# Kernel tuning notes

Measured on AMD Instinct MI355X. Metric: run time of the kernel, lower is better.

## Reference

```python
import jax, jax.numpy as jnp
import numpy as np

SMOOTH = 1e-05
NUM_CLASSES = 2  # binary segmentation labels {0,1}


def setup_inputs() -> dict:
    key = jax.random.key(0)
    k1, k2 = jax.random.split(key)
    shape = (32, 1, 1024, 1024)
    input = jax.random.normal(k1, shape, dtype=jnp.float32)
    target = jax.random.randint(k2, shape, 0, NUM_CLASSES, dtype=jnp.int32)
    return {"input": input, "target": target}


def reference(input, target):
    # sigmoid probabilities, flattened
    p = jax.nn.sigmoid(input).reshape(-1)
    t_int = target.reshape(-1)
    t = t_int.astype(p.dtype)

    # class-frequency histogram (fixed length -> jit-compatible)
    class_frequencies = jnp.bincount(t_int, length=NUM_CLASSES)
    class_weights = 1.0 / (class_frequencies.astype(p.dtype) + SMOOTH) ** 2
    w = class_weights[t_int]  # gather per-pixel weight

    intersection = jnp.sum(w * p * t)
    denominator = jnp.sum(w * (p * p + t * t))
    dice_loss = 1.0 - (2.0 * intersection + SMOOTH) / (denominator + SMOOTH)
    return dice_loss
```

## Files before the change

kernel.cpp:

```cpp
#include <hip/hip_runtime.h>

#define SMOOTH 1e-5

typedef float f32x4 __attribute__((ext_vector_type(4)));
typedef int   i32x4 __attribute__((ext_vector_type(4)));

__device__ __forceinline__ f32x4 ldnt(const f32x4* p) {
    return __builtin_nontemporal_load(p);
}

__global__ __launch_bounds__(256, 8) void balanced_loss_stage1(
    const float* __restrict__ in, const int* __restrict__ tg,
    long long n, double* __restrict__ ws)
{
    const long long nvec = n >> 2;
    float lc1 = 0.f, ls1 = 0.f, lqa = 0.f, lq1 = 0.f;

    const long long tid    = (long long)blockIdx.x * blockDim.x + threadIdx.x;
    const long long stride = (long long)gridDim.x * blockDim.x;
    const f32x4* __restrict__ in4 = (const f32x4*)in;
    const i32x4* __restrict__ tg4 = (const i32x4*)tg;

#define PROC(xv, tv)                                        \
    {                                                       \
        float e  = __expf(-(xv));                           \
        float p  = __builtin_amdgcn_rcpf(1.f + e);          \
        float pp = p * p;                                   \
        float ft = (float)(tv);             \
        lqa += pp;                                          \
        lc1 += ft;                                          \
        ls1 += ft * p;                                      \
        lq1 += ft * pp;                                     \
    }

    long long i = tid;
    for (; i + 3 * stride < nvec; i += 4 * stride) {
        f32x4 x0 = ldnt(in4 + i);
        i32x4 t0 = tg4[i];
        f32x4 x1 = ldnt(in4 + i + stride);
        i32x4 t1 = tg4[i + stride];
        f32x4 x2 = ldnt(in4 + i + 2 * stride);
        i32x4 t2 = tg4[i + 2 * stride];
        f32x4 x3 = ldnt(in4 + i + 3 * stride);
        i32x4 t3 = tg4[i + 3 * stride];
        __builtin_amdgcn_sched_barrier(0);
        PROC(x0.x, t0.x); PROC(x0.y, t0.y); PROC(x0.z, t0.z); PROC(x0.w, t0.w);
        PROC(x1.x, t1.x); PROC(x1.y, t1.y); PROC(x1.z, t1.z); PROC(x1.w, t1.w);
        PROC(x2.x, t2.x); PROC(x2.y, t2.y); PROC(x2.z, t2.z); PROC(x2.w, t2.w);
        PROC(x3.x, t3.x); PROC(x3.y, t3.y); PROC(x3.z, t3.z); PROC(x3.w, t3.w);
    }
    for (; i < nvec; i += stride) {
        f32x4 x = ldnt(in4 + i);
        i32x4 t = tg4[i];
        PROC(x.x, t.x); PROC(x.y, t.y); PROC(x.z, t.z); PROC(x.w, t.w);
    }

    const long long tail0 = nvec << 2;
    if (blockIdx.x == 0) {
        for (long long j = tail0 + threadIdx.x; j < n; j += blockDim.x) {
            float x = in[j];
            int   t = tg[j];
            PROC(x, t);
        }
    }
#undef PROC

    double dc1 = (double)lc1, ds1 = (double)ls1;
    double dqa = (double)lqa, dq1 = (double)lq1;
    for (int off = 32; off > 0; off >>= 1) {
        dc1 += __shfl_down(dc1, off, 64);
        ds1 += __shfl_down(ds1, off, 64);
        dqa += __shfl_down(dqa, off, 64);
        dq1 += __shfl_down(dq1, off, 64);
    }

    __shared__ double sm[4][4];
    const int wid  = threadIdx.x >> 6;
    const int lane = threadIdx.x & 63;
    if (lane == 0) {
        sm[wid][0] = dc1; sm[wid][1] = ds1;
        sm[wid][2] = dqa; sm[wid][3] = dq1;
    }
    __syncthreads();
    if (threadIdx.x == 0) {
        double a0 = 0, a1 = 0, a2 = 0, a3 = 0;
        for (int w = 0; w < 4; ++w) {
            a0 += sm[w][0]; a1 += sm[w][1];
            a2 += sm[w][2]; a3 += sm[w][3];
        }
        double* p = ws + (size_t)blockIdx.x * 4;
        p[0] = a0; p[1] = a1; p[2] = a2; p[3] = a3;
    }
}

__global__ __launch_bounds__(1024) void balanced_loss_stage2(
    const double* __restrict__ ws, int nblocks,
    float* __restrict__ out, long long n)
{
    double c1 = 0, s1 = 0, qa = 0, q1 = 0;
    for (int b = threadIdx.x; b < nblocks; b += blockDim.x) {
        const double* p = ws + (size_t)b * 4;
        c1 += p[0]; s1 += p[1]; qa += p[2]; q1 += p[3];
    }
    for (int off = 32; off > 0; off >>= 1) {
        c1 += __shfl_down(c1, off, 64);
        s1 += __shfl_down(s1, off, 64);
        qa += __shfl_down(qa, off, 64);
        q1 += __shfl_down(q1, off, 64);
    }
    __shared__ double sm[16][4];
    const int wid  = threadIdx.x >> 6;
    const int lane = threadIdx.x & 63;
    if (lane == 0) {
        sm[wid][0] = c1; sm[wid][1] = s1;
        sm[wid][2] = qa; sm[wid][3] = q1;
    }
    __syncthreads();
    if (threadIdx.x == 0) {
        double a0 = 0, a1 = 0, a2 = 0, a3 = 0;
        const int nw = blockDim.x >> 6;
        for (int w = 0; w < nw; ++w) {
            a0 += sm[w][0]; a1 += sm[w][1];
            a2 += sm[w][2]; a3 += sm[w][3];
        }
        double cc1 = a0;
        double cc0 = (double)n - cc1;
        double w0 = 1.0 / ((cc0 + SMOOTH) * (cc0 + SMOOTH));
        double w1 = 1.0 / ((cc1 + SMOOTH) * (cc1 + SMOOTH));
        double q0 = a2 - a3;
        double I  = w1 * a1;
        double D  = w0 * q0 + w1 * (a3 + cc1);
        out[0] = (float)(1.0 - (2.0 * I + SMOOTH) / (D + SMOOTH));
    }
}

extern "C" void kernel_launch(void* const* d_in, const int* in_sizes, int n_in,
                              void* d_out, int out_size, void* d_ws, size_t ws_size,
                              hipStream_t stream) {
    const float* in = (const float*)d_in[0];
    const int*   tg = (const int*)d_in[1];
    long long n = (long long)in_sizes[0];
    double* ws = (double*)d_ws;

    const int block = 256;
    const int grid  = 2048;

    balanced_loss_stage1<<<grid, block, 0, stream>>>(in, tg, n, ws);
    balanced_loss_stage2<<<1, 1024, 0, stream>>>(ws, grid, (float*)d_out, n);
}
```

Baseline: 51.07 us.

## Double-buffer global loads in stage1 and halve grid with 32-bit indexing

Stage1 now uses two register sets, so the next group of four vector loads is issued before the current group is processed. This software pipelining aims to hide memory latency inside each thread. Indices switch from 64-bit to 32-bit to cut address arithmetic, and the grid drops to 1024 blocks with launch bounds relaxed to 4 waves per SIMD to leave room for the extra registers. The cost is lower occupancy and more register pressure, which could reduce overall memory-level parallelism.

```diff
diff --git a/kernel.cpp b/kernel.cpp
--- a/kernel.cpp
+++ b/kernel.cpp
@@ -9,15 +9,15 @@
     return __builtin_nontemporal_load(p);
 }
 
-__global__ __launch_bounds__(256, 8) void balanced_loss_stage1(
+__global__ __launch_bounds__(256, 4) void balanced_loss_stage1(
     const float* __restrict__ in, const int* __restrict__ tg,
     long long n, double* __restrict__ ws)
 {
-    const long long nvec = n >> 2;
+    const int nvec = (int)(n >> 2);
     float lc1 = 0.f, ls1 = 0.f, lqa = 0.f, lq1 = 0.f;
 
-    const long long tid    = (long long)blockIdx.x * blockDim.x + threadIdx.x;
-    const long long stride = (long long)gridDim.x * blockDim.x;
+    const int tid    = blockIdx.x * blockDim.x + threadIdx.x;
+    const int stride = gridDim.x * blockDim.x;
     const f32x4* __restrict__ in4 = (const f32x4*)in;
     const i32x4* __restrict__ tg4 = (const i32x4*)tg;
 
@@ -32,30 +32,51 @@
         ls1 += ft * p;                                      \
         lq1 += ft * pp;                                     \
     }
+#define PROC4(X, T) { PROC((X).x, (T).x); PROC((X).y, (T).y); PROC((X).z, (T).z); PROC((X).w, (T).w); }
 
-    long long i = tid;
-    for (; i + 3 * stride < nvec; i += 4 * stride) {
-        f32x4 x0 = ldnt(in4 + i);
-        i32x4 t0 = tg4[i];
-        f32x4 x1 = ldnt(in4 + i + stride);
-        i32x4 t1 = tg4[i + stride];
-        f32x4 x2 = ldnt(in4 + i + 2 * stride);
-        i32x4 t2 = tg4[i + 2 * stride];
-        f32x4 x3 = ldnt(in4 + i + 3 * stride);
-        i32x4 t3 = tg4[i + 3 * stride];
-        __builtin_amdgcn_sched_barrier(0);
-        PROC(x0.x, t0.x); PROC(x0.y, t0.y); PROC(x0.z, t0.z); PROC(x0.w, t0.w);
-        PROC(x1.x, t1.x); PROC(x1.y, t1.y); PROC(x1.z, t1.z); PROC(x1.w, t1.w);
-        PROC(x2.x, t2.x); PROC(x2.y, t2.y); PROC(x2.z, t2.z); PROC(x2.w, t2.w);
-        PROC(x3.x, t3.x); PROC(x3.y, t3.y); PROC(x3.z, t3.z); PROC(x3.w, t3.w);
+#define LOADG(X0,X1,X2,X3, T0,T1,T2,T3, base)               \
+    {                                                       \
+        int b0 = (base), b1 = b0 + stride;                  \
+        int b2 = b1 + stride, b3 = b2 + stride;             \
+        X0 = ldnt(in4 + b0);  T0 = tg4[b0];                 \
+        X1 = ldnt(in4 + b1);  T1 = tg4[b1];                 \
+        X2 = ldnt(in4 + b2);  T2 = tg4[b2];                 \
+        X3 = ldnt(in4 + b3);  T3 = tg4[b3];                 \
+        __builtin_amdgcn_sched_barrier(0);                  \
+    }
+
+    int i = tid;
+    const int stride4 = 4 * stride;
+    f32x4 xa0, xa1, xa2, xa3, xb0, xb1, xb2, xb3;
+    i32x4 ta0, ta1, ta2, ta3, tb0, tb1, tb2, tb3;
+
+    if (i + 3 * stride < nvec) {
+        LOADG(xa0,xa1,xa2,xa3, ta0,ta1,ta2,ta3, i);
+        i += stride4;
+        for (;;) {
+            if (i + 3 * stride >= nvec) {
+                PROC4(xa0, ta0); PROC4(xa1, ta1); PROC4(xa2, ta2); PROC4(xa3, ta3);
+                break;
+            }
+            LOADG(xb0,xb1,xb2,xb3, tb0,tb1,tb2,tb3, i);
+            i += stride4;
+            PROC4(xa0, ta0); PROC4(xa1, ta1); PROC4(xa2, ta2); PROC4(xa3, ta3);
+            if (i + 3 * stride >= nvec) {
+                PROC4(xb0, tb0); PROC4(xb1, tb1); PROC4(xb2, tb2); PROC4(xb3, tb3);
+                break;
+            }
+            LOADG(xa0,xa1,xa2,xa3, ta0,ta1,ta2,ta3, i);
+            i += stride4;
+            PROC4(xb0, tb0); PROC4(xb1, tb1); PROC4(xb2, tb2); PROC4(xb3, tb3);
+        }
     }
     for (; i < nvec; i += stride) {
         f32x4 x = ldnt(in4 + i);
         i32x4 t = tg4[i];
-        PROC(x.x, t.x); PROC(x.y, t.y); PROC(x.z, t.z); PROC(x.w, t.w);
+        PROC4(x, t);
     }
 
-    const long long tail0 = nvec << 2;
+    const long long tail0 = (long long)nvec << 2;
     if (blockIdx.x == 0) {
         for (long long j = tail0 + threadIdx.x; j < n; j += blockDim.x) {
             float x = in[j];
@@ -63,6 +84,8 @@
             PROC(x, t);
         }
     }
+#undef LOADG
+#undef PROC4
 #undef PROC
 
     double dc1 = (double)lc1, ds1 = (double)ls1;
@@ -143,7 +166,7 @@
     double* ws = (double*)d_ws;
 
     const int block = 256;
-    const int grid  = 2048;
+    const int grid  = 1024;
 
     balanced_loss_stage1<<<grid, block, 0, stream>>>(in, tg, n, ws);
     balanced_loss_stage2<<<1, 1024, 0, stream>>>(ws, grid, (float*)d_out, n);
```

New measurement: 52.42 us. +2.7%, slower.
